# Performance work log

Measured on AMD Instinct MI355X. Metric: run time of the kernel, lower is better.

The kernel has to match this reference:

```python
import jax, jax.numpy as jnp
import numpy as np

HIDDEN = 768
PDIM = int(HIDDEN / 4.67)  # 164
QK_DIM = 16
EPS = 1e-5


def setup_inputs() -> dict:
    key = jax.random.key(0)
    k_hs, k_qkv, k_out = jax.random.split(key, 3)
    B, S = 8, 2048
    hidden_states = jax.random.normal(k_hs, (B, S, HIDDEN), dtype=jnp.float32)
    qkv_out = 2 * QK_DIM + PDIM  # 196
    qkv_w = jax.random.normal(k_qkv, (qkv_out, PDIM), dtype=jnp.float32) * (PDIM ** -0.5)
    qkv_b = jnp.zeros((qkv_out,), dtype=jnp.float32)
    out_w = jax.random.normal(k_out, (HIDDEN, HIDDEN), dtype=jnp.float32) * (HIDDEN ** -0.5)
    out_b = jnp.zeros((HIDDEN,), dtype=jnp.float32)
    ln_scale = jnp.ones((PDIM,), dtype=jnp.float32)
    ln_bias = jnp.zeros((PDIM,), dtype=jnp.float32)
    return {
        "hidden_states": hidden_states,
        "ln_scale": ln_scale,
        "ln_bias": ln_bias,
        "qkv_w": qkv_w,
        "qkv_b": qkv_b,
        "out_w": out_w,
        "out_b": out_b,
    }


def reference(hidden_states, ln_scale, ln_bias, qkv_w, qkv_b, out_w, out_b):
    # channel split
    x1 = hidden_states[..., :PDIM]   # [B,S,pdim]
    x2 = hidden_states[..., PDIM:]   # [B,S,hidden-pdim]
    # LayerNorm over last dim
    mean = jnp.mean(x1, axis=-1, keepdims=True)
    var = jnp.mean(jnp.square(x1 - mean), axis=-1, keepdims=True)
    x1n = (x1 - mean) * jax.lax.rsqrt(var + EPS) * ln_scale + ln_bias
    # qkv projection: [B,S,2*qk+pdim]
    qkv = jnp.einsum("bsd,od->bso", x1n, qkv_w) + qkv_b
    q = qkv[..., :QK_DIM]
    k = qkv[..., QK_DIM:2 * QK_DIM]
    v = qkv[..., 2 * QK_DIM:]
    scale = QK_DIM ** -0.5
    scores = jnp.einsum("bqd,bkd->bqk", q, k) * scale  # [B,S,S]
    probs = jax.nn.softmax(scores, axis=-1)
    attended = jnp.einsum("bqk,bkd->bqd", probs, v)  # [B,S,pdim]
    merged = jnp.concatenate([attended, x2], axis=-1)  # [B,S,hidden]
    out = jnp.einsum("bsd,od->bso", merged, out_w) + out_b
    return out
```

## Files before the change

### kernel.cpp

```cpp
#include <hip/hip_runtime.h>
#include <hip/hip_bf16.h>

#define HID 768
#define PD 164
#define NQ 196
#define SEQ 2048

typedef __attribute__((ext_vector_type(8))) short bf16x8_t;
typedef __attribute__((ext_vector_type(4))) float f32x4_t;
typedef __attribute__((ext_vector_type(16))) float f32x16_t;
typedef __attribute__((ext_vector_type(4))) unsigned int u32x4_t;

static __device__ __forceinline__ unsigned short f2bfu(float f) {
  union { __hip_bfloat16 h; unsigned short u; } cv;
  cv.h = __float2bfloat16(f);
  return cv.u;
}

static __device__ __forceinline__ unsigned cvtpk(float a, float b) {
  unsigned r;
  asm("v_cvt_pk_bf16_f32 %0, %1, %2" : "=v"(r) : "v"(a), "v"(b));
  return r;
}

static __device__ __forceinline__ void gload16(const void* g, void* l) {
  __builtin_amdgcn_global_load_lds(
      (const __attribute__((address_space(1))) void*)g,
      (__attribute__((address_space(3))) void*)l, 16, 0, 0);
}

__global__ __launch_bounds__(256) void k_prep(const float* __restrict__ qkv_w,
                                              const float* __restrict__ out_w,
                                              unsigned short* __restrict__ qwb,
                                              unsigned short* __restrict__ wb) {
  int bid = blockIdx.x;
  if (bid < 576) {
    int i = (bid * 256 + threadIdx.x) * 4;
    float4 v = *(const float4*)(out_w + i);
    ushort4 o;
    o.x = f2bfu(v.x); o.y = f2bfu(v.y); o.z = f2bfu(v.z); o.w = f2bfu(v.w);
    *(ushort4*)(wb + i) = o;
  } else {
    int i = ((bid - 576) * 256 + threadIdx.x) * 4;
    int n = i / 192, k = i - n * 192;
    float v0 = (n < NQ && k + 0 < PD) ? qkv_w[n * PD + k + 0] : 0.f;
    float v1 = (n < NQ && k + 1 < PD) ? qkv_w[n * PD + k + 1] : 0.f;
    float v2 = (n < NQ && k + 2 < PD) ? qkv_w[n * PD + k + 2] : 0.f;
    float v3 = (n < NQ && k + 3 < PD) ? qkv_w[n * PD + k + 3] : 0.f;
    ushort4 o;
    o.x = f2bfu(v0); o.y = f2bfu(v1); o.z = f2bfu(v2); o.w = f2bfu(v3);
    *(ushort4*)(qwb + i) = o;
  }
}

__global__ __launch_bounds__(256, 2) void k_lnqkv(const float* __restrict__ hidden,
                                                  const float* __restrict__ lns,
                                                  const float* __restrict__ lnb,
                                                  const unsigned short* __restrict__ qwb,
                                                  const float* __restrict__ qkv_b,
                                                  unsigned short* __restrict__ merged,
                                                  unsigned short* __restrict__ qg,
                                                  unsigned short* __restrict__ kg,
                                                  unsigned short* __restrict__ v16) {
  __shared__ float xr[64][172];
  __shared__ float stats[64][2];
  __shared__ unsigned short Aq[64][200];
  int t = threadIdx.x;
  int r0 = blockIdx.x * 64;
  #pragma unroll
  for (int i = 0; i < 11; i++) {
    int idx = t + i * 256;
    if (idx < 2624) {
      int row = idx / 41, q = idx - row * 41;
      float4 v = *(const float4*)(hidden + (size_t)(r0 + row) * HID + q * 4);
      *(float4*)&xr[row][q * 4] = v;
    }
  }
  __syncthreads();
  {
    int l = t & 63, w = t >> 6;
    int row = w * 16 + (l & 15), g = l >> 4;
    float sum = 0.f, sq = 0.f;
    #pragma unroll
    for (int j = 0; j < 41; j++) {
      float x = xr[row][g * 41 + j];
      sum += x; sq += x * x;
    }
    sum += __shfl_xor(sum, 16, 64); sum += __shfl_xor(sum, 32, 64);
    sq  += __shfl_xor(sq, 16, 64);  sq  += __shfl_xor(sq, 32, 64);
    float mean = sum * (1.f / PD);
    float var = sq * (1.f / PD) - mean * mean;
    float rstd = rsqrtf(var + 1e-5f);
    if (g == 0) { stats[row][0] = mean; stats[row][1] = rstd; }
  }
  __syncthreads();
  #pragma unroll
  for (int i = 0; i < 24; i++) {
    int idx = t + i * 256;
    int row = idx / 96, c2 = idx - row * 96;
    int d = c2 * 2;
    float mean = stats[row][0], rstd = stats[row][1];
    float v0 = (d < PD)     ? (xr[row][d]     - mean) * rstd * lns[d]     + lnb[d]     : 0.f;
    float v1 = (d + 1 < PD) ? (xr[row][d + 1] - mean) * rstd * lns[d + 1] + lnb[d + 1] : 0.f;
    unsigned int pk = (unsigned int)f2bfu(v0) | ((unsigned int)f2bfu(v1) << 16);
    *(unsigned int*)(&Aq[row][d]) = pk;
  }
  #pragma unroll
  for (int i = 0; i < 38; i++) {
    int idx = t + i * 256;
    if (idx < 9664) {
      int row = idx / 151, q = idx - row * 151;
      int d = PD + q * 4;
      float4 v = *(const float4*)(hidden + (size_t)(r0 + row) * HID + d);
      ushort4 o;
      o.x = f2bfu(v.x); o.y = f2bfu(v.y); o.z = f2bfu(v.z); o.w = f2bfu(v.w);
      *(ushort4*)(merged + (size_t)(r0 + row) * HID + d) = o;
    }
  }
  __syncthreads();
  int l = t & 63, w = t >> 6, lr15 = l & 15, g = l >> 4;
  f32x4_t acc[13];
  #pragma unroll
  for (int n = 0; n < 13; n++) acc[n] = (f32x4_t){0.f, 0.f, 0.f, 0.f};
  #pragma unroll 2
  for (int kc = 0; kc < 6; kc++) {
    bf16x8_t a = *(const bf16x8_t*)(&Aq[w * 16 + lr15][kc * 32 + g * 8]);
    #pragma unroll
    for (int n = 0; n < 13; n++) {
      bf16x8_t b = *(const bf16x8_t*)(qwb + (size_t)(n * 16 + lr15) * 192 + kc * 32 + g * 8);
      acc[n] = __builtin_amdgcn_mfma_f32_16x16x32_bf16(a, b, acc[n], 0, 0, 0);
    }
  }
  {
    float bias = qkv_b[lr15];
    #pragma unroll
    for (int r = 0; r < 4; r++) {
      int grow = r0 + w * 16 + g * 4 + r;
      qg[(size_t)grow * 16 + lr15] = f2bfu((acc[0][r] + bias) * 0.36067376022224085f);
    }
  }
  {
    float bias = qkv_b[16 + lr15];
    #pragma unroll
    for (int r = 0; r < 4; r++) {
      int grow = r0 + w * 16 + g * 4 + r;
      kg[(size_t)grow * 16 + lr15] = f2bfu(acc[1][r] + bias);
    }
  }
  int s0 = (r0 & 2047) + w * 16;
  int bb = r0 >> 11;
  size_t vrowbase = (size_t)(bb * 128 + (s0 >> 4)) * 192;
  #pragma unroll
  for (int n = 2; n < 13; n++) {
    int col = n * 16 + lr15;
    int d = col - 32;
    float bias = (col < NQ) ? qkv_b[col] : 0.f;
    float v0 = acc[n][0] + bias, v1 = acc[n][1] + bias;
    float v2 = acc[n][2] + bias, v3 = acc[n][3] + bias;
    if (d == 164) { v0 = v1 = v2 = v3 = 1.f; }
    else if (d >= PD) { v0 = v1 = v2 = v3 = 0.f; }
    ushort4 o;
    o.x = f2bfu(v0); o.y = f2bfu(v1); o.z = f2bfu(v2); o.w = f2bfu(v3);
    *(ushort4*)(v16 + (vrowbase + d) * 16 + g * 4) = o;
  }
}

__global__ __launch_bounds__(256, 2) void k_attn(const unsigned short* __restrict__ qg,
                                                 const unsigned short* __restrict__ kg,
                                                 const unsigned short* __restrict__ v16,
                                                 unsigned short* __restrict__ merged) {
  __shared__ float red[2][64 * 98];
  int t = threadIdx.x;
  int w = t >> 6, l = t & 63;
  int b = blockIdx.x & 7, qt = blockIdx.x >> 3;
  int lo = l & 31, hi = l >> 5;
  int qbase = b * SEQ + qt * 32;
  bf16x8_t qf = *(const bf16x8_t*)(qg + (size_t)(qbase + lo) * 16 + hi * 8);
  const unsigned short* kb = kg + (size_t)b * SEQ * 16;
  const unsigned short* vbb = v16 + (size_t)b * 128 * 192 * 16;
  f32x16_t zro;
  #pragma unroll
  for (int r = 0; r < 16; r++) zro[r] = 0.f;
  f32x16_t acc[6];
  #pragma unroll
  for (int f = 0; f < 6; f++) acc[f] = zro;

  int it0 = w * 8;
  bf16x8_t kf0 = *(const bf16x8_t*)(kb + (size_t)(it0 * 64 + lo) * 16 + hi * 8);
  bf16x8_t kf1 = *(const bf16x8_t*)(kb + (size_t)(it0 * 64 + 32 + lo) * 16 + hi * 8);
  bf16x8_t va[6], vb_[6];
  {
    const unsigned short* vt0 = vbb + (size_t)(it0 * 4) * (192 * 16) + hi * 8;
    #pragma unroll
    for (int f = 0; f < 6; f++) va[f] = *(const bf16x8_t*)(vt0 + (f * 32 + lo) * 16);
  }
  for (int it = it0; it < it0 + 8; ++it) {
    bf16x8_t nk0 = *(const bf16x8_t*)(kb + (size_t)((it + 1) * 64 + lo) * 16 + hi * 8);
    bf16x8_t nk1 = *(const bf16x8_t*)(kb + (size_t)((it + 1) * 64 + 32 + lo) * 16 + hi * 8);
    f32x16_t sc0 = __builtin_amdgcn_mfma_f32_32x32x16_bf16(kf0, qf, zro, 0, 0, 0);
    f32x16_t sc1 = __builtin_amdgcn_mfma_f32_32x32x16_bf16(kf1, qf, zro, 0, 0, 0);
    bf16x8_t pa[4];
    #pragma unroll
    for (int jt = 0; jt < 2; ++jt) {
      f32x16_t sc = jt ? sc1 : sc0;
      unsigned u[8];
      #pragma unroll
      for (int k = 0; k < 8; ++k)
        u[k] = cvtpk(exp2f(sc[2 * k]), exp2f(sc[2 * k + 1]));
      asm volatile("v_permlane32_swap_b32 %0, %1" : "+v"(u[0]), "+v"(u[2]));
      asm volatile("v_permlane32_swap_b32 %0, %1" : "+v"(u[1]), "+v"(u[3]));
      asm volatile("v_permlane32_swap_b32 %0, %1" : "+v"(u[4]), "+v"(u[6]));
      asm volatile("v_permlane32_swap_b32 %0, %1" : "+v"(u[5]), "+v"(u[7]));
      union { u32x4_t u4; bf16x8_t h8; } c0, c1;
      c0.u4 = (u32x4_t){u[0], u[1], u[2], u[3]};
      c1.u4 = (u32x4_t){u[4], u[5], u[6], u[7]};
      pa[jt * 2 + 0] = c0.h8;
      pa[jt * 2 + 1] = c1.h8;
    }
#define PV_STEP(JS, VCUR, VNXT, NT, NJS)                                            \
    {                                                                               \
      const unsigned short* vtn = vbb + (size_t)((NT) * 4 + (NJS)) * (192 * 16) + hi * 8; \
      _Pragma("unroll")                                                             \
      for (int f = 0; f < 6; f++) VNXT[f] = *(const bf16x8_t*)(vtn + (f * 32 + lo) * 16); \
      _Pragma("unroll")                                                             \
      for (int f = 0; f < 6; f++)                                                   \
        acc[f] = __builtin_amdgcn_mfma_f32_32x32x16_bf16(pa[JS], VCUR[f], acc[f], 0, 0, 0); \
    }
    PV_STEP(0, va,  vb_, it, 1)
    PV_STEP(1, vb_, va,  it, 2)
    PV_STEP(2, va,  vb_, it, 3)
    PV_STEP(3, vb_, va,  it + 1, 0)
#undef PV_STEP
    kf0 = nk0; kf1 = nk1;
  }

  if (w >= 2) {
    float* dst = &red[w - 2][l * 98];
    #pragma unroll
    for (int f = 0; f < 6; f++)
      #pragma unroll
      for (int r = 0; r < 16; r += 2)
        *(float2*)(dst + f * 16 + r) = make_float2(acc[f][r], acc[f][r + 1]);
  }
  __syncthreads();
  if (w < 2) {
    const float* src = &red[w][l * 98];
    #pragma unroll
    for (int f = 0; f < 6; f++)
      #pragma unroll
      for (int r = 0; r < 16; r += 2) {
        float2 v = *(const float2*)(src + f * 16 + r);
        acc[f][r] += v.x; acc[f][r + 1] += v.y;
      }
  }
  __syncthreads();
  if (w == 1) {
    float* dst = &red[0][l * 98];
    #pragma unroll
    for (int f = 0; f < 6; f++)
      #pragma unroll
      for (int r = 0; r < 16; r += 2)
        *(float2*)(dst + f * 16 + r) = make_float2(acc[f][r], acc[f][r + 1]);
  }
  __syncthreads();
  if (w == 0) {
    const float* src = &red[0][l * 98];
    #pragma unroll
    for (int f = 0; f < 6; f++)
      #pragma unroll
      for (int r = 0; r < 16; r += 2) {
        float2 v = *(const float2*)(src + f * 16 + r);
        acc[f][r] += v.x; acc[f][r + 1] += v.y;
      }
    float dninv[16];
    #pragma unroll
    for (int r = 0; r < 16; ++r)
      dninv[r] = 1.0f / __shfl(acc[5][r], 4 + hi * 32, 64);
    #pragma unroll
    for (int f = 0; f < 6; ++f) {
      int d = f * 32 + lo;
      if (d < PD) {
        #pragma unroll
        for (int r = 0; r < 16; ++r) {
          int q = qbase + (r & 3) + 8 * (r >> 2) + 4 * hi;
          merged[(size_t)q * HID + d] = f2bfu(acc[f][r] * dninv[r]);
        }
      }
    }
  }
}

__global__ __launch_bounds__(256, 3) void k_out(const unsigned short* __restrict__ mg,
                                                const unsigned short* __restrict__ wb,
                                                const float* __restrict__ out_b,
                                                float* __restrict__ out) {
  __shared__ unsigned short Al[2][128 * 32];
  __shared__ unsigned short Bl[2][128 * 32];
  int t = threadIdx.x;
  int bid = blockIdx.x;
  int wgid = (bid & 7) * 96 + (bid >> 3);
  int nb = wgid % 6, mb = wgid / 6;
  int m0 = mb * 128, n0 = nb * 128;
  int l = t & 63, w = t >> 6, wr = w >> 1, wc = w & 1;
  int lr = l & 15, lg = l >> 4;
  int sw = (lr >> 1) & 3;
  f32x4_t acc[4][4];
  #pragma unroll
  for (int mi = 0; mi < 4; mi++)
    #pragma unroll
    for (int ni = 0; ni < 4; ni++) acc[mi][ni] = (f32x4_t){0.f, 0.f, 0.f, 0.f};

  auto stage = [&](int buf, int kt) {
    #pragma unroll
    for (int i = 0; i < 2; i++) {
      int off = t + i * 256;
      int row = off >> 2, c = off & 3;
      int cs = c ^ ((row >> 1) & 3);
      gload16(mg + (size_t)(m0 + row) * HID + kt * 32 + cs * 8, (char*)&Al[buf][0] + off * 16);
    }
    #pragma unroll
    for (int i = 0; i < 2; i++) {
      int off = t + i * 256;
      int row = off >> 2, c = off & 3;
      int cs = c ^ ((row >> 1) & 3);
      gload16(wb + (size_t)(n0 + row) * HID + kt * 32 + cs * 8, (char*)&Bl[buf][0] + off * 16);
    }
  };
  auto compute = [&](int cur) {
    __builtin_amdgcn_s_setprio(1);
    bf16x8_t a[4], bfr[4];
    int slot = lg ^ sw;
    #pragma unroll
    for (int mi = 0; mi < 4; mi++)
      a[mi] = *(const bf16x8_t*)(&Al[cur][(wr * 64 + mi * 16 + lr) * 32 + slot * 8]);
    #pragma unroll
    for (int ni = 0; ni < 4; ni++)
      bfr[ni] = *(const bf16x8_t*)(&Bl[cur][(wc * 64 + ni * 16 + lr) * 32 + slot * 8]);
    #pragma unroll
    for (int mi = 0; mi < 4; mi++)
      #pragma unroll
      for (int ni = 0; ni < 4; ni++)
        acc[mi][ni] = __builtin_amdgcn_mfma_f32_16x16x32_bf16(a[mi], bfr[ni], acc[mi][ni], 0, 0, 0);
    __builtin_amdgcn_s_setprio(0);
  };

  stage(0, 0);
  stage(1, 1);
  for (int kt = 0; kt < 23; kt++) {
    int cur = kt & 1;
    asm volatile("s_waitcnt vmcnt(4)" ::: "memory");
    __builtin_amdgcn_sched_barrier(0);
    __builtin_amdgcn_s_barrier();
    compute(cur);
    asm volatile("s_waitcnt lgkmcnt(0)" ::: "memory");
    __builtin_amdgcn_sched_barrier(0);
    __builtin_amdgcn_s_barrier();
    if (kt + 2 < 24) stage(cur, kt + 2);
  }
  asm volatile("s_waitcnt vmcnt(0)" ::: "memory");
  __builtin_amdgcn_sched_barrier(0);
  __builtin_amdgcn_s_barrier();
  compute(1);

  #pragma unroll
  for (int ni = 0; ni < 4; ni++) {
    int col = n0 + wc * 64 + ni * 16 + lr;
    float bias = out_b[col];
    #pragma unroll
    for (int mi = 0; mi < 4; mi++) {
      #pragma unroll
      for (int r = 0; r < 4; r++) {
        int row = m0 + wr * 64 + mi * 16 + lg * 4 + r;
        out[(size_t)row * HID + col] = acc[mi][ni][r] + bias;
      }
    }
  }
}

extern "C" void kernel_launch(void* const* d_in, const int* in_sizes, int n_in,
                              void* d_out, int out_size, void* d_ws, size_t ws_size,
                              hipStream_t stream) {
  const float* hidden = (const float*)d_in[0];
  const float* lns    = (const float*)d_in[1];
  const float* lnb    = (const float*)d_in[2];
  const float* qkv_w  = (const float*)d_in[3];
  const float* qkv_b  = (const float*)d_in[4];
  const float* out_w  = (const float*)d_in[5];
  const float* out_b  = (const float*)d_in[6];
  char* ws = (char*)d_ws;
  unsigned short* qg  = (unsigned short*)(ws + 0);
  unsigned short* kg  = (unsigned short*)(ws + 524288);
  unsigned short* v16 = (unsigned short*)(ws + 1048576);
  unsigned short* qwb = (unsigned short*)(ws + 13631488);
  unsigned short* wb  = (unsigned short*)(ws + 13711360);
  unsigned short* mg  = (unsigned short*)(ws + 14891008);
  hipLaunchKernelGGL(k_prep,  dim3(615), dim3(256), 0, stream, qkv_w, out_w, qwb, wb);
  hipLaunchKernelGGL(k_lnqkv, dim3(256), dim3(256), 0, stream, hidden, lns, lnb, qwb, qkv_b,
                     mg, qg, kg, v16);
  hipLaunchKernelGGL(k_attn,  dim3(512), dim3(256), 0, stream, qg, kg, v16, mg);
  hipLaunchKernelGGL(k_out,   dim3(768), dim3(256), 0, stream, mg, wb, out_b, (float*)d_out);
}
```

Baseline: 96.82 us.

## Split attention PV output dimension across wave pairs with 512-thread blocks

The attention kernel now runs 8 waves per block instead of 4. Each pair of waves shares a key range and splits the 192-wide V dimension in halves, so each wave holds 3 accumulators instead of 6. The cross-wave reduction and the denominator broadcast are rewritten to go through shared memory. This cuts register pressure and raises occupancy, but every QK^T MFMA and exp is now computed twice, once per half, and the K/V prefetch across iterations is dropped.

```diff
diff --git a/kernel.cpp b/kernel.cpp
--- a/kernel.cpp
+++ b/kernel.cpp
@@ -165,13 +165,16 @@
   }
 }
 
-__global__ __launch_bounds__(256, 2) void k_attn(const unsigned short* __restrict__ qg,
+__global__ __launch_bounds__(512, 4) void k_attn(const unsigned short* __restrict__ qg,
                                                  const unsigned short* __restrict__ kg,
                                                  const unsigned short* __restrict__ v16,
                                                  unsigned short* __restrict__ merged) {
-  __shared__ float red[2][64 * 98];
+  __shared__ float red[4][64 * 50];
+  __shared__ float sl[2][16];
   int t = threadIdx.x;
   int w = t >> 6, l = t & 63;
+  int dh = w & 1, jq = w >> 1;
+  int dh3 = dh * 3;
   int b = blockIdx.x & 7, qt = blockIdx.x >> 3;
   int lo = l & 31, hi = l >> 5;
   int qbase = b * SEQ + qt * 32;
@@ -181,32 +184,28 @@
   f32x16_t zro;
   #pragma unroll
   for (int r = 0; r < 16; r++) zro[r] = 0.f;
-  f32x16_t acc[6];
-  #pragma unroll
-  for (int f = 0; f < 6; f++) acc[f] = zro;
-
-  int it0 = w * 8;
-  bf16x8_t kf0 = *(const bf16x8_t*)(kb + (size_t)(it0 * 64 + lo) * 16 + hi * 8);
-  bf16x8_t kf1 = *(const bf16x8_t*)(kb + (size_t)(it0 * 64 + 32 + lo) * 16 + hi * 8);
-  bf16x8_t va[6], vb_[6];
-  {
-    const unsigned short* vt0 = vbb + (size_t)(it0 * 4) * (192 * 16) + hi * 8;
-    #pragma unroll
-    for (int f = 0; f < 6; f++) va[f] = *(const bf16x8_t*)(vt0 + (f * 32 + lo) * 16);
-  }
+  f32x16_t acc[3];
+  #pragma unroll
+  for (int f = 0; f < 3; f++) acc[f] = zro;
+
+  int it0 = jq * 8;
   for (int it = it0; it < it0 + 8; ++it) {
-    bf16x8_t nk0 = *(const bf16x8_t*)(kb + (size_t)((it + 1) * 64 + lo) * 16 + hi * 8);
-    bf16x8_t nk1 = *(const bf16x8_t*)(kb + (size_t)((it + 1) * 64 + 32 + lo) * 16 + hi * 8);
+    bf16x8_t kf0 = *(const bf16x8_t*)(kb + (size_t)(it * 64 + lo) * 16 + hi * 8);
+    bf16x8_t kf1 = *(const bf16x8_t*)(kb + (size_t)(it * 64 + 32 + lo) * 16 + hi * 8);
+    bf16x8_t va[3], vb_[3];
+    {
+      const unsigned short* vt0 = vbb + (size_t)(it * 4) * (192 * 16) + hi * 8;
+      #pragma unroll
+      for (int f = 0; f < 3; f++) va[f] = *(const bf16x8_t*)(vt0 + ((dh3 + f) * 32 + lo) * 16);
+    }
     f32x16_t sc0 = __builtin_amdgcn_mfma_f32_32x32x16_bf16(kf0, qf, zro, 0, 0, 0);
     f32x16_t sc1 = __builtin_amdgcn_mfma_f32_32x32x16_bf16(kf1, qf, zro, 0, 0, 0);
     bf16x8_t pa[4];
-    #pragma unroll
-    for (int jt = 0; jt < 2; ++jt) {
-      f32x16_t sc = jt ? sc1 : sc0;
+    {
       unsigned u[8];
       #pragma unroll
       for (int k = 0; k < 8; ++k)
-        u[k] = cvtpk(exp2f(sc[2 * k]), exp2f(sc[2 * k + 1]));
+        u[k] = cvtpk(exp2f(sc0[2 * k]), exp2f(sc0[2 * k + 1]));
       asm volatile("v_permlane32_swap_b32 %0, %1" : "+v"(u[0]), "+v"(u[2]));
       asm volatile("v_permlane32_swap_b32 %0, %1" : "+v"(u[1]), "+v"(u[3]));
       asm volatile("v_permlane32_swap_b32 %0, %1" : "+v"(u[4]), "+v"(u[6]));
@@ -214,71 +213,97 @@
       union { u32x4_t u4; bf16x8_t h8; } c0, c1;
       c0.u4 = (u32x4_t){u[0], u[1], u[2], u[3]};
       c1.u4 = (u32x4_t){u[4], u[5], u[6], u[7]};
-      pa[jt * 2 + 0] = c0.h8;
-      pa[jt * 2 + 1] = c1.h8;
-    }
-#define PV_STEP(JS, VCUR, VNXT, NT, NJS)                                            \
+      pa[0] = c0.h8; pa[1] = c1.h8;
+    }
+    {
+      unsigned u[8];
+      #pragma unroll
+      for (int k = 0; k < 8; ++k)
+        u[k] = cvtpk(exp2f(sc1[2 * k]), exp2f(sc1[2 * k + 1]));
+      asm volatile("v_permlane32_swap_b32 %0, %1" : "+v"(u[0]), "+v"(u[2]));
+      asm volatile("v_permlane32_swap_b32 %0, %1" : "+v"(u[1]), "+v"(u[3]));
+      asm volatile("v_permlane32_swap_b32 %0, %1" : "+v"(u[4]), "+v"(u[6]));
+      asm volatile("v_permlane32_swap_b32 %0, %1" : "+v"(u[5]), "+v"(u[7]));
+      union { u32x4_t u4; bf16x8_t h8; } c0, c1;
+      c0.u4 = (u32x4_t){u[0], u[1], u[2], u[3]};
+      c1.u4 = (u32x4_t){u[4], u[5], u[6], u[7]};
+      pa[2] = c0.h8; pa[3] = c1.h8;
+    }
+#define PV_STEP(JS, VCUR, VNXT, PREF)                                               \
     {                                                                               \
-      const unsigned short* vtn = vbb + (size_t)((NT) * 4 + (NJS)) * (192 * 16) + hi * 8; \
+      if (PREF) {                                                                   \
+        const unsigned short* vtn = vbb + (size_t)(it * 4 + (JS) + 1) * (192 * 16) + hi * 8; \
+        _Pragma("unroll")                                                           \
+        for (int f = 0; f < 3; f++) VNXT[f] = *(const bf16x8_t*)(vtn + ((dh3 + f) * 32 + lo) * 16); \
+      }                                                                             \
       _Pragma("unroll")                                                             \
-      for (int f = 0; f < 6; f++) VNXT[f] = *(const bf16x8_t*)(vtn + (f * 32 + lo) * 16); \
-      _Pragma("unroll")                                                             \
-      for (int f = 0; f < 6; f++)                                                   \
+      for (int f = 0; f < 3; f++)                                                   \
         acc[f] = __builtin_amdgcn_mfma_f32_32x32x16_bf16(pa[JS], VCUR[f], acc[f], 0, 0, 0); \
     }
-    PV_STEP(0, va,  vb_, it, 1)
-    PV_STEP(1, vb_, va,  it, 2)
-    PV_STEP(2, va,  vb_, it, 3)
-    PV_STEP(3, vb_, va,  it + 1, 0)
+    PV_STEP(0, va,  vb_, 1)
+    PV_STEP(1, vb_, va,  1)
+    PV_STEP(2, va,  vb_, 1)
+    PV_STEP(3, vb_, va,  0)
 #undef PV_STEP
-    kf0 = nk0; kf1 = nk1;
-  }
-
-  if (w >= 2) {
-    float* dst = &red[w - 2][l * 98];
-    #pragma unroll
-    for (int f = 0; f < 6; f++)
+  }
+
+  if (jq >= 2) {
+    float* dst = &red[(jq - 2) * 2 + dh][l * 50];
+    #pragma unroll
+    for (int f = 0; f < 3; f++)
       #pragma unroll
       for (int r = 0; r < 16; r += 2)
         *(float2*)(dst + f * 16 + r) = make_float2(acc[f][r], acc[f][r + 1]);
   }
   __syncthreads();
-  if (w < 2) {
-    const float* src = &red[w][l * 98];
-    #pragma unroll
-    for (int f = 0; f < 6; f++)
+  if (jq <= 1) {
+    const float* src = &red[jq * 2 + dh][l * 50];
+    #pragma unroll
+    for (int f = 0; f < 3; f++)
       #pragma unroll
       for (int r = 0; r < 16; r += 2) {
         float2 v = *(const float2*)(src + f * 16 + r);
         acc[f][r] += v.x; acc[f][r + 1] += v.y;
       }
   }
-  __syncthreads();
-  if (w == 1) {
-    float* dst = &red[0][l * 98];
-    #pragma unroll
-    for (int f = 0; f < 6; f++)
+  if (jq == 1) {
+    float* dst = &red[2 + dh][l * 50];
+    #pragma unroll
+    for (int f = 0; f < 3; f++)
       #pragma unroll
       for (int r = 0; r < 16; r += 2)
         *(float2*)(dst + f * 16 + r) = make_float2(acc[f][r], acc[f][r + 1]);
   }
   __syncthreads();
-  if (w == 0) {
-    const float* src = &red[0][l * 98];
-    #pragma unroll
-    for (int f = 0; f < 6; f++)
+  float dninv[16];
+  if (jq == 0) {
+    const float* src = &red[2 + dh][l * 50];
+    #pragma unroll
+    for (int f = 0; f < 3; f++)
       #pragma unroll
       for (int r = 0; r < 16; r += 2) {
         float2 v = *(const float2*)(src + f * 16 + r);
         acc[f][r] += v.x; acc[f][r + 1] += v.y;
       }
-    float dninv[16];
-    #pragma unroll
-    for (int r = 0; r < 16; ++r)
-      dninv[r] = 1.0f / __shfl(acc[5][r], 4 + hi * 32, 64);
-    #pragma unroll
-    for (int f = 0; f < 6; ++f) {
-      int d = f * 32 + lo;
+    if (dh == 1) {
+      #pragma unroll
+      for (int r = 0; r < 16; ++r)
+        dninv[r] = 1.0f / __shfl(acc[2][r], 4 + hi * 32, 64);
+      if (lo == 0) {
+        #pragma unroll
+        for (int r = 0; r < 16; ++r) sl[hi][r] = dninv[r];
+      }
+    }
+  }
+  __syncthreads();
+  if (jq == 0) {
+    if (dh == 0) {
+      #pragma unroll
+      for (int r = 0; r < 16; ++r) dninv[r] = sl[hi][r];
+    }
+    #pragma unroll
+    for (int f = 0; f < 3; ++f) {
+      int d = (dh3 + f) * 32 + lo;
       if (d < PD) {
         #pragma unroll
         for (int r = 0; r < 16; ++r) {
@@ -397,6 +422,6 @@
   hipLaunchKernelGGL(k_prep,  dim3(615), dim3(256), 0, stream, qkv_w, out_w, qwb, wb);
   hipLaunchKernelGGL(k_lnqkv, dim3(256), dim3(256), 0, stream, hidden, lns, lnb, qwb, qkv_b,
                      mg, qg, kg, v16);
-  hipLaunchKernelGGL(k_attn,  dim3(512), dim3(256), 0, stream, qg, kg, v16, mg);
+  hipLaunchKernelGGL(k_attn,  dim3(512), dim3(512), 0, stream, qg, kg, v16, mg);
   hipLaunchKernelGGL(k_out,   dim3(768), dim3(256), 0, stream, mg, wb, out_b, (float*)d_out);
 }
```

Result: slower. 101.3 us (+4.7%).
